# Kernel optimization log

Hardware: AMD Instinct MI355X
Metric: run time of the kernel (lower is better)

Reference implementation:

```python
import jax, jax.numpy as jnp
import numpy as np

TEMPERATURE = 8.0  # sqrt(d_k) with d_k = 64


def setup_inputs() -> dict:
    key = jax.random.key(0)
    kq, kk, kv, km = jax.random.split(key, 4)
    B, S, D = 32, 2048, 64
    q = jax.random.normal(kq, (B, S, D), dtype=jnp.float32)
    k = jax.random.normal(kk, (B, S, D), dtype=jnp.float32)
    v = jax.random.normal(kv, (B, S, D), dtype=jnp.float32)
    mask = jax.random.randint(km, (B, S, S), 0, 2).astype(jnp.bool_)
    return {"q": q, "k": k, "v": v, "mask": mask}


def reference(q, k, v, mask):
    # scores: [B, S, S] = q @ k^T, mask -> -inf, scale by 1/temperature
    scores = jnp.einsum("bqd,bkd->bqk", q, k)
    scores = jnp.where(mask, -jnp.inf, scores) / TEMPERATURE
    attn = jax.nn.softmax(scores, axis=2)
    output = jnp.einsum("bqk,bkd->bqd", attn, v)
    return (output, attn)
```

## Files before the change

kernel.cpp:

```cpp
#include <hip/hip_runtime.h>
#include <hip/hip_bf16.h>

typedef __attribute__((ext_vector_type(8))) short short8;
typedef __attribute__((ext_vector_type(4))) short short4b;
typedef __attribute__((ext_vector_type(4))) float f32x4;

#define S_LEN 2048
#define DIM   64
#define NB    32
#define BR    64
#define BC    64
#define NKT   (S_LEN / BC)

#define KP  72
#define BP  33
#define AP  68

__device__ __forceinline__ short f2bf(float f) {
    __hip_bfloat16 h = __float2bfloat16(f);
    return __builtin_bit_cast(short, h);
}

__device__ __forceinline__ void barrier_raw() {
    __builtin_amdgcn_sched_barrier(0);
    __builtin_amdgcn_s_barrier();
    __builtin_amdgcn_sched_barrier(0);
}
__device__ __forceinline__ void barrier_pub() {
    __builtin_amdgcn_sched_barrier(0);
    asm volatile("s_waitcnt lgkmcnt(0)" ::: "memory");
    __builtin_amdgcn_s_barrier();
    __builtin_amdgcn_sched_barrier(0);
}


__global__ __launch_bounds__(256)
void conv_k_kernel(const float* __restrict__ k, short* __restrict__ kbf)
{
    size_t idx = ((size_t)blockIdx.x * 256 + threadIdx.x) * 8;
    const float* p = k + idx;
    float4 a = *(const float4*)p;
    float4 c = *(const float4*)(p + 4);
    short8 f;
    f[0]=f2bf(a.x); f[1]=f2bf(a.y); f[2]=f2bf(a.z); f[3]=f2bf(a.w);
    f[4]=f2bf(c.x); f[5]=f2bf(c.y); f[6]=f2bf(c.z); f[7]=f2bf(c.w);
    *(short8*)(kbf + idx) = f;
}

__global__ __launch_bounds__(256)
void conv_vt_kernel(const float* __restrict__ v, short* __restrict__ vtb)
{
    __shared__ float tile[64][65];
    const int t  = threadIdx.x;
    const int b  = blockIdx.x >> 5;
    const int j0 = (blockIdx.x & 31) * 64;

    #pragma unroll
    for (int p = 0; p < 4; ++p) {
        int j = (t >> 4) + p * 16;
        int d = (t & 15) * 4;
        float4 x = *(const float4*)(v + ((size_t)(b * S_LEN + j0 + j) * DIM + d));
        tile[j][d+0]=x.x; tile[j][d+1]=x.y; tile[j][d+2]=x.z; tile[j][d+3]=x.w;
    }
    __syncthreads();
    #pragma unroll
    for (int p = 0; p < 4; ++p) {
        int d  = (t >> 4) + p * 16;
        int j4 = (t & 15) * 4;
        short4b s4;
        s4[0]=f2bf(tile[j4+0][d]); s4[1]=f2bf(tile[j4+1][d]);
        s4[2]=f2bf(tile[j4+2][d]); s4[3]=f2bf(tile[j4+3][d]);
        *(short4b*)(vtb + ((size_t)(b * DIM + d) * S_LEN + j0 + j4)) = s4;
    }
}


__global__ __launch_bounds__(256, 4)
void sdpa_v8(const float* __restrict__ q, const int* __restrict__ mask,
             const short* __restrict__ kbf, const short* __restrict__ vtb,
             float* __restrict__ out, float* __restrict__ attn)
{
    __shared__ __align__(16) short Klds[BR * KP];
    __shared__ __align__(16) short Vtlds[DIM * KP];
    __shared__ __align__(16) float Albs[BR * AP];

    const int t  = threadIdx.x;
    const int l  = t & 63;
    const int wv = t >> 6;
    const int lg = l >> 4;
    const int ll = l & 15;

    const int bx  = blockIdx.x;
    const int kk  = bx >> 3;
    const int b   = (bx & 7) * 4 + (kk >> 5);
    const int i0  = (kk & 31) * BR;

    const float LOG2E_T = 0.18033688011112042f;

    const int krow = t >> 2;
    const int kcol = (t & 3) * 16;
    const size_t kgbase = (size_t)(b * S_LEN + krow) * DIM + kcol;
    const size_t vgbase = (size_t)(b * DIM + krow) * S_LEN + kcol;
    const size_t mbase  = (size_t)(b * S_LEN + i0 + 16 * wv) * S_LEN + l;

    short8 qf[2];
    {
        const float* qrow = q + ((size_t)(b * S_LEN + i0 + 16 * wv + ll) * DIM);
        #pragma unroll
        for (int s = 0; s < 2; ++s) {
            const float* p = qrow + s * 32 + lg * 8;
            float4 a = *(const float4*)p;
            float4 c = *(const float4*)(p + 4);
            short8 f;
            f[0]=f2bf(a.x); f[1]=f2bf(a.y); f[2]=f2bf(a.z); f[3]=f2bf(a.w);
            f[4]=f2bf(c.x); f[5]=f2bf(c.y); f[6]=f2bf(c.z); f[7]=f2bf(c.w);
            qf[s] = f;
        }
    }

    short8 kA0 = *(const short8*)(kbf + kgbase);
    short8 kA1 = *(const short8*)(kbf + kgbase + 8);
    int mA[16], mB[16];
    #pragma unroll
    for (int r = 0; r < 16; ++r)
        mA[r] = __builtin_nontemporal_load(mask + mbase + (size_t)r * S_LEN);
    #pragma unroll
    for (int r = 0; r < 16; ++r)
        mB[r] = __builtin_nontemporal_load(mask + mbase + BC + (size_t)r * S_LEN);

    float rs[4] = {0.f, 0.f, 0.f, 0.f};
    unsigned long long w8[8];

    for (int o = 0; o < 4; ++o) {
        #pragma unroll
        for (int u = 0; u < 8; ++u) {
            const int kt = 8 * o + u;
            int (&cur)[16] = (u & 1) ? mB : mA;

            unsigned long long wb[4];
            #pragma unroll
            for (int r = 0; r < 16; ++r) {
                unsigned long long bal = __ballot(cur[r] != 0);
                if ((r >> 2) == lg) wb[r & 3] = bal;
                if (lg == o && ll == r) w8[u] = bal;
            }

            barrier_raw();
            {
                short* kd = &Klds[krow * KP + kcol];
                *(short8*)kd = kA0;
                *(short8*)(kd + 8) = kA1;
            }
            barrier_pub();

            {
                const int ktn = (kt < NKT - 1) ? kt + 1 : kt;
                const short* kb = kbf + kgbase + (size_t)ktn * BC * DIM;
                kA0 = *(const short8*)kb;
                kA1 = *(const short8*)(kb + 8);
                const int kt2 = (kt < NKT - 2) ? kt + 2 : kt;
                const int* mrow = mask + mbase + (size_t)kt2 * BC;
                #pragma unroll
                for (int r = 0; r < 16; ++r)
                    cur[r] = __builtin_nontemporal_load(mrow + (size_t)r * S_LEN);
            }
            __builtin_amdgcn_sched_barrier(0);

            #pragma unroll
            for (int jt = 0; jt < 4; ++jt) {
                short8 b0 = *(short8*)&Klds[(jt * 16 + ll) * KP + lg * 8];
                short8 b1 = *(short8*)&Klds[(jt * 16 + ll) * KP + 32 + lg * 8];
                f32x4 c = {0.f, 0.f, 0.f, 0.f};
                c = __builtin_amdgcn_mfma_f32_16x16x32_bf16(qf[0], b0, c, 0, 0, 0);
                c = __builtin_amdgcn_mfma_f32_16x16x32_bf16(qf[1], b1, c, 0, 0, 0);
                #pragma unroll
                for (int r = 0; r < 4; ++r) {
                    unsigned int bit = (unsigned int)(wb[r] >> (jt * 16 + ll)) & 1u;
                    rs[r] += bit ? 0.f : __builtin_amdgcn_exp2f(c[r] * LOG2E_T);
                }
            }
        }
    }

    kA0 = *(const short8*)(kbf + kgbase);
    kA1 = *(const short8*)(kbf + kgbase + 8);
    short8 vA0 = *(const short8*)(vtb + vgbase);
    short8 vA1 = *(const short8*)(vtb + vgbase + 8);

    float inv[4];
    #pragma unroll
    for (int r = 0; r < 4; ++r) {
        float s = rs[r];
        s += __shfl_xor(s, 1);
        s += __shfl_xor(s, 2);
        s += __shfl_xor(s, 4);
        s += __shfl_xor(s, 8);
        inv[r] = 1.0f / s;
    }

    f32x4 oacc[4];
    #pragma unroll
    for (int dt = 0; dt < 4; ++dt) oacc[dt] = (f32x4){0.f, 0.f, 0.f, 0.f};

    float* const abase = attn + (size_t)b * S_LEN * S_LEN;

    for (int o = 0; o < 4; ++o) {
        #pragma unroll
        for (int u = 0; u < 8; ++u) {
            const int kt = 8 * o + u;
            const int j0 = kt * BC;

            barrier_raw();
            {
                short* kd = &Klds[krow * KP + kcol];
                *(short8*)kd = kA0;
                *(short8*)(kd + 8) = kA1;
                short* vd = &Vtlds[krow * KP + kcol];
                *(short8*)vd = vA0;
                *(short8*)(vd + 8) = vA1;
            }
            barrier_pub();

            {
                const int ktn = (kt < NKT - 1) ? kt + 1 : kt;
                const short* kb = kbf + kgbase + (size_t)ktn * BC * DIM;
                kA0 = *(const short8*)kb;
                kA1 = *(const short8*)(kb + 8);
                const short* vb = vtb + vgbase + (size_t)ktn * BC;
                vA0 = *(const short8*)vb;
                vA1 = *(const short8*)(vb + 8);
            }
            __builtin_amdgcn_sched_barrier(0);

            unsigned long long wb[4];
            #pragma unroll
            for (int r = 0; r < 4; ++r)
                wb[r] = __shfl(w8[u], 16 * o + lg * 4 + r);

            #pragma unroll
            for (int jt = 0; jt < 4; ++jt) {
                short8 b0 = *(short8*)&Klds[(jt * 16 + ll) * KP + lg * 8];
                short8 b1 = *(short8*)&Klds[(jt * 16 + ll) * KP + 32 + lg * 8];
                f32x4 c = {0.f, 0.f, 0.f, 0.f};
                c = __builtin_amdgcn_mfma_f32_16x16x32_bf16(qf[0], b0, c, 0, 0, 0);
                c = __builtin_amdgcn_mfma_f32_16x16x32_bf16(qf[1], b1, c, 0, 0, 0);
                #pragma unroll
                for (int r = 0; r < 4; ++r) {
                    unsigned int bit = (unsigned int)(wb[r] >> (jt * 16 + ll)) & 1u;
                    float pexp = bit ? 0.f : __builtin_amdgcn_exp2f(c[r] * LOG2E_T);
                    Albs[(16 * wv + lg * 4 + r) * AP + jt * 16 + ll] = pexp * inv[r];
                }
            }

            short8 paf[2];
            #pragma unroll
            for (int s = 0; s < 2; ++s) {
                const float* ap = &Albs[(16 * wv + ll) * AP + s * 32 + lg * 8];
                float4 x = *(const float4*)ap;
                float4 y = *(const float4*)(ap + 4);
                short8 f;
                f[0]=f2bf(x.x); f[1]=f2bf(x.y); f[2]=f2bf(x.z); f[3]=f2bf(x.w);
                f[4]=f2bf(y.x); f[5]=f2bf(y.y); f[6]=f2bf(y.z); f[7]=f2bf(y.w);
                paf[s] = f;
            }

            #pragma unroll
            for (int dt = 0; dt < 4; ++dt) {
                short8 b0 = *(short8*)&Vtlds[(dt * 16 + ll) * KP + lg * 8];
                short8 b1 = *(short8*)&Vtlds[(dt * 16 + ll) * KP + 32 + lg * 8];
                oacc[dt] = __builtin_amdgcn_mfma_f32_16x16x32_bf16(paf[0], b0, oacc[dt], 0, 0, 0);
                oacc[dt] = __builtin_amdgcn_mfma_f32_16x16x32_bf16(paf[1], b1, oacc[dt], 0, 0, 0);
            }

            #pragma unroll
            for (int ps = 0; ps < 4; ++ps) {
                int row = 16 * wv + lg + ps * 4;
                f32x4 val = *(f32x4*)&Albs[row * AP + ll * 4];
                float* dst = abase + (size_t)(i0 + row) * S_LEN + j0 + ll * 4;
                __builtin_nontemporal_store(val, (f32x4*)dst);
            }
        }
    }

    #pragma unroll
    for (int dt = 0; dt < 4; ++dt)
        #pragma unroll
        for (int r = 0; r < 4; ++r)
            out[(size_t)(b * S_LEN + i0 + 16 * wv + lg * 4 + r) * DIM + dt * 16 + ll] = oacc[dt][r];
}


__global__ __launch_bounds__(256, 3)
void sdpa_fb(const float* __restrict__ q, const float* __restrict__ k,
             const float* __restrict__ v, const int* __restrict__ mask,
             float* __restrict__ out, float* __restrict__ attn)
{
    __shared__ __align__(16) short Klds[BR * KP];
    __shared__ __align__(16) short Vtlds[DIM * KP];
    __shared__ __align__(16) unsigned long long Bits[BR * BP];
    __shared__ __align__(16) float Albs[BR * AP];

    const int t  = threadIdx.x;
    const int l  = t & 63;
    const int wv = t >> 6;
    const int lg = l >> 4;
    const int ll = l & 15;

    const int wg = blockIdx.x;
    const int b  = wg >> 5;
    const int i0 = (wg & 31) * BR;

    const float LOG2E_T = 0.18033688011112042f;

    short8 qf[2];
    {
        const float* qrow = q + ((size_t)(b * S_LEN + i0 + 16 * wv + ll) * DIM);
        #pragma unroll
        for (int s = 0; s < 2; ++s) {
            const float* p = qrow + s * 32 + lg * 8;
            float4 a = *(const float4*)p;
            float4 c = *(const float4*)(p + 4);
            short8 f;
            f[0]=f2bf(a.x); f[1]=f2bf(a.y); f[2]=f2bf(a.z); f[3]=f2bf(a.w);
            f[4]=f2bf(c.x); f[5]=f2bf(c.y); f[6]=f2bf(c.z); f[7]=f2bf(c.w);
            qf[s] = f;
        }
    }

    float rs[4] = {0.f, 0.f, 0.f, 0.f};

    for (int kt = 0; kt < NKT; ++kt) {
        const int j0 = kt * BC;
        #pragma unroll
        for (int p = 0; p < 4; ++p) {
            int row = (t >> 4) + p * 16;
            int dd  = (t & 15) * 4;
            float4 kv4 = *(const float4*)(k + ((size_t)(b * S_LEN + j0 + row) * DIM + dd));
            short4b s4;
            s4[0]=f2bf(kv4.x); s4[1]=f2bf(kv4.y); s4[2]=f2bf(kv4.z); s4[3]=f2bf(kv4.w);
            *(short4b*)&Klds[row * KP + dd] = s4;
        }
        {
            const int* mrow = mask + (size_t)(b * S_LEN + i0 + 16 * wv) * S_LEN + j0 + l;
            int mv[16];
            #pragma unroll
            for (int r = 0; r < 16; ++r)
                mv[r] = __builtin_nontemporal_load(mrow + (size_t)r * S_LEN);
            unsigned long long myword = 0ull;
            #pragma unroll
            for (int r = 0; r < 16; ++r) {
                unsigned long long bal = __ballot(mv[r] != 0);
                if (ll == r) myword = bal;
            }
            if (l < 16) Bits[(16 * wv + l) * BP + kt] = myword;
        }
        __syncthreads();

        unsigned long long wbits[4];
        #pragma unroll
        for (int r = 0; r < 4; ++r)
            wbits[r] = Bits[(16 * wv + lg * 4 + r) * BP + kt];

        #pragma unroll
        for (int jt = 0; jt < 4; ++jt) {
            short8 b0 = *(short8*)&Klds[(jt * 16 + ll) * KP + lg * 8];
            short8 b1 = *(short8*)&Klds[(jt * 16 + ll) * KP + 32 + lg * 8];
            f32x4 c = {0.f, 0.f, 0.f, 0.f};
            c = __builtin_amdgcn_mfma_f32_16x16x32_bf16(qf[0], b0, c, 0, 0, 0);
            c = __builtin_amdgcn_mfma_f32_16x16x32_bf16(qf[1], b1, c, 0, 0, 0);
            #pragma unroll
            for (int r = 0; r < 4; ++r) {
                unsigned int bit = (unsigned int)(wbits[r] >> (jt * 16 + ll)) & 1u;
                rs[r] += bit ? 0.f : __builtin_amdgcn_exp2f(c[r] * LOG2E_T);
            }
        }
        __syncthreads();
    }

    float inv[4];
    #pragma unroll
    for (int r = 0; r < 4; ++r) {
        float s = rs[r];
        s += __shfl_xor(s, 1);
        s += __shfl_xor(s, 2);
        s += __shfl_xor(s, 4);
        s += __shfl_xor(s, 8);
        inv[r] = 1.0f / s;
    }

    f32x4 oacc[4];
    #pragma unroll
    for (int dt = 0; dt < 4; ++dt) oacc[dt] = (f32x4){0.f, 0.f, 0.f, 0.f};

    for (int kt = 0; kt < NKT; ++kt) {
        const int j0 = kt * BC;
        #pragma unroll
        for (int p = 0; p < 4; ++p) {
            int row = (t >> 4) + p * 16;
            int dd  = (t & 15) * 4;
            float4 kv4 = *(const float4*)(k + ((size_t)(b * S_LEN + j0 + row) * DIM + dd));
            short4b s4;
            s4[0]=f2bf(kv4.x); s4[1]=f2bf(kv4.y); s4[2]=f2bf(kv4.z); s4[3]=f2bf(kv4.w);
            *(short4b*)&Klds[row * KP + dd] = s4;
        }
        #pragma unroll
        for (int it = 0; it < 8; ++it) {
            int jp = (t >> 4) + (it & 1) * 16;
            int dd = (t & 15) + (it >> 1) * 16;
            const float* vp = v + ((size_t)(b * S_LEN + j0 + jp * 2) * DIM + dd);
            float v0 = vp[0];
            float v1 = vp[DIM];
            unsigned int pk = (unsigned int)(unsigned short)f2bf(v0) |
                              ((unsigned int)(unsigned short)f2bf(v1) << 16);
            *(unsigned int*)&Vtlds[dd * KP + jp * 2] = pk;
        }
        __syncthreads();

        unsigned long long wbits[4];
        #pragma unroll
        for (int r = 0; r < 4; ++r)
            wbits[r] = Bits[(16 * wv + lg * 4 + r) * BP + kt];

        #pragma unroll
        for (int jt = 0; jt < 4; ++jt) {
            short8 b0 = *(short8*)&Klds[(jt * 16 + ll) * KP + lg * 8];
            short8 b1 = *(short8*)&Klds[(jt * 16 + ll) * KP + 32 + lg * 8];
            f32x4 c = {0.f, 0.f, 0.f, 0.f};
            c = __builtin_amdgcn_mfma_f32_16x16x32_bf16(qf[0], b0, c, 0, 0, 0);
            c = __builtin_amdgcn_mfma_f32_16x16x32_bf16(qf[1], b1, c, 0, 0, 0);
            #pragma unroll
            for (int r = 0; r < 4; ++r) {
                unsigned int bit = (unsigned int)(wbits[r] >> (jt * 16 + ll)) & 1u;
                float pexp = bit ? 0.f : __builtin_amdgcn_exp2f(c[r] * LOG2E_T);
                Albs[(16 * wv + lg * 4 + r) * AP + jt * 16 + ll] = pexp * inv[r];
            }
        }

        short8 paf[2];
        #pragma unroll
        for (int s = 0; s < 2; ++s) {
            const float* ap = &Albs[(16 * wv + ll) * AP + s * 32 + lg * 8];
            float4 x = *(const float4*)ap;
            float4 y = *(const float4*)(ap + 4);
            short8 f;
            f[0]=f2bf(x.x); f[1]=f2bf(x.y); f[2]=f2bf(x.z); f[3]=f2bf(x.w);
            f[4]=f2bf(y.x); f[5]=f2bf(y.y); f[6]=f2bf(y.z); f[7]=f2bf(y.w);
            paf[s] = f;
        }

        #pragma unroll
        for (int dt = 0; dt < 4; ++dt) {
            short8 b0 = *(short8*)&Vtlds[(dt * 16 + ll) * KP + lg * 8];
            short8 b1 = *(short8*)&Vtlds[(dt * 16 + ll) * KP + 32 + lg * 8];
            oacc[dt] = __builtin_amdgcn_mfma_f32_16x16x32_bf16(paf[0], b0, oacc[dt], 0, 0, 0);
            oacc[dt] = __builtin_amdgcn_mfma_f32_16x16x32_bf16(paf[1], b1, oacc[dt], 0, 0, 0);
        }

        {
            float* abase = attn + (size_t)b * S_LEN * S_LEN;
            #pragma unroll
            for (int ps = 0; ps < 4; ++ps) {
                int row = 16 * wv + lg + ps * 4;
                f32x4 val = *(f32x4*)&Albs[row * AP + ll * 4];
                float* dst = abase + (size_t)(i0 + row) * S_LEN + j0 + ll * 4;
                __builtin_nontemporal_store(val, (f32x4*)dst);
            }
        }
        __syncthreads();
    }

    #pragma unroll
    for (int dt = 0; dt < 4; ++dt)
        #pragma unroll
        for (int r = 0; r < 4; ++r)
            out[(size_t)(b * S_LEN + i0 + 16 * wv + lg * 4 + r) * DIM + dt * 16 + ll] = oacc[dt][r];
}

extern "C" void kernel_launch(void* const* d_in, const int* in_sizes, int n_in,
                              void* d_out, int out_size, void* d_ws, size_t ws_size,
                              hipStream_t stream) {
    const float* q    = (const float*)d_in[0];
    const float* k    = (const float*)d_in[1];
    const float* v    = (const float*)d_in[2];
    const int*   mask = (const int*)d_in[3];
    float* out  = (float*)d_out;
    float* attn = out + (size_t)NB * S_LEN * DIM;

    const size_t nel = (size_t)NB * S_LEN * DIM;
    const size_t ws_needed = 2 * nel * sizeof(short);

    if (ws_size >= ws_needed) {
        short* kbf = (short*)d_ws;
        short* vtb = kbf + nel;
        conv_k_kernel<<<dim3(nel / (256 * 8)), dim3(256), 0, stream>>>(k, kbf);
        conv_vt_kernel<<<dim3(NB * 32), dim3(256), 0, stream>>>(v, vtb);
        sdpa_v8<<<dim3(NB * (S_LEN / BR)), dim3(256), 0, stream>>>(q, mask, kbf, vtb, out, attn);
    } else {
        sdpa_fb<<<dim3(NB * (S_LEN / BR)), dim3(256), 0, stream>>>(q, k, v, mask, out, attn);
    }
}
```

Before: 305.2 us.

## Process key tiles in pairs with explicit A/B register double-buffering

Both passes now step through the key dimension two 64-column tiles at a time, holding K (and V) prefetches in separate A/B register sets instead of reusing one set with a clamped index. The mask prefetch is restructured to load a 128-column strip (both halves) per step. In the output pass, the attn stores for both tiles are buffered in registers and written together as adjacent 128-column row segments. The aim is to keep more loads in flight and to coalesce the global attn writes, at the cost of higher register pressure under launch_bounds(256,4).

```diff
diff --git a/kernel.cpp b/kernel.cpp
--- a/kernel.cpp
+++ b/kernel.cpp
@@ -76,7 +76,7 @@
 
 
 __global__ __launch_bounds__(256, 4)
-void sdpa_v8(const float* __restrict__ q, const int* __restrict__ mask,
+void sdpa_v9(const float* __restrict__ q, const int* __restrict__ mask,
              const short* __restrict__ kbf, const short* __restrict__ vtb,
              float* __restrict__ out, float* __restrict__ attn)
 {
@@ -120,29 +120,32 @@
 
     short8 kA0 = *(const short8*)(kbf + kgbase);
     short8 kA1 = *(const short8*)(kbf + kgbase + 8);
-    int mA[16], mB[16];
-    #pragma unroll
-    for (int r = 0; r < 16; ++r)
-        mA[r] = __builtin_nontemporal_load(mask + mbase + (size_t)r * S_LEN);
-    #pragma unroll
-    for (int r = 0; r < 16; ++r)
-        mB[r] = __builtin_nontemporal_load(mask + mbase + BC + (size_t)r * S_LEN);
+    short8 kB0, kB1;
+    int m[32];
+    #pragma unroll
+    for (int r = 0; r < 16; ++r) {
+        m[2*r+0] = __builtin_nontemporal_load(mask + mbase + (size_t)r * S_LEN);
+        m[2*r+1] = __builtin_nontemporal_load(mask + mbase + (size_t)r * S_LEN + 64);
+    }
 
     float rs[4] = {0.f, 0.f, 0.f, 0.f};
     unsigned long long w8[8];
 
     for (int o = 0; o < 4; ++o) {
         #pragma unroll
-        for (int u = 0; u < 8; ++u) {
-            const int kt = 8 * o + u;
-            int (&cur)[16] = (u & 1) ? mB : mA;
-
-            unsigned long long wb[4];
+        for (int ss = 0; ss < 4; ++ss) {
+            const int kt0 = 8 * o + 2 * ss;
+            const int sI  = 4 * o + ss;
+
+            unsigned long long wb[2][4];
             #pragma unroll
             for (int r = 0; r < 16; ++r) {
-                unsigned long long bal = __ballot(cur[r] != 0);
-                if ((r >> 2) == lg) wb[r & 3] = bal;
-                if (lg == o && ll == r) w8[u] = bal;
+                #pragma unroll
+                for (int h = 0; h < 2; ++h) {
+                    unsigned long long bal = __ballot(m[2*r+h] != 0);
+                    if ((r >> 2) == lg) wb[h][r & 3] = bal;
+                    if (lg == o && ll == r) w8[2*ss+h] = bal;
+                }
             }
 
             barrier_raw();
@@ -152,20 +155,19 @@
                 *(short8*)(kd + 8) = kA1;
             }
             barrier_pub();
-
             {
-                const int ktn = (kt < NKT - 1) ? kt + 1 : kt;
-                const short* kb = kbf + kgbase + (size_t)ktn * BC * DIM;
-                kA0 = *(const short8*)kb;
-                kA1 = *(const short8*)(kb + 8);
-                const int kt2 = (kt < NKT - 2) ? kt + 2 : kt;
-                const int* mrow = mask + mbase + (size_t)kt2 * BC;
-                #pragma unroll
-                for (int r = 0; r < 16; ++r)
-                    cur[r] = __builtin_nontemporal_load(mrow + (size_t)r * S_LEN);
+                const short* kb = kbf + kgbase + (size_t)(kt0 + 1) * BC * DIM;
+                kB0 = *(const short8*)kb;
+                kB1 = *(const short8*)(kb + 8);
+                const int sN = (sI < 15) ? sI + 1 : sI;
+                const int* mp = mask + mbase + (size_t)sN * 128;
+                #pragma unroll
+                for (int r = 0; r < 16; ++r) {
+                    m[2*r+0] = __builtin_nontemporal_load(mp + (size_t)r * S_LEN);
+                    m[2*r+1] = __builtin_nontemporal_load(mp + (size_t)r * S_LEN + 64);
+                }
             }
             __builtin_amdgcn_sched_barrier(0);
-
             #pragma unroll
             for (int jt = 0; jt < 4; ++jt) {
                 short8 b0 = *(short8*)&Klds[(jt * 16 + ll) * KP + lg * 8];
@@ -175,7 +177,35 @@
                 c = __builtin_amdgcn_mfma_f32_16x16x32_bf16(qf[1], b1, c, 0, 0, 0);
                 #pragma unroll
                 for (int r = 0; r < 4; ++r) {
-                    unsigned int bit = (unsigned int)(wb[r] >> (jt * 16 + ll)) & 1u;
+                    unsigned int bit = (unsigned int)(wb[0][r] >> (jt * 16 + ll)) & 1u;
+                    rs[r] += bit ? 0.f : __builtin_amdgcn_exp2f(c[r] * LOG2E_T);
+                }
+            }
+
+            barrier_raw();
+            {
+                short* kd = &Klds[krow * KP + kcol];
+                *(short8*)kd = kB0;
+                *(short8*)(kd + 8) = kB1;
+            }
+            barrier_pub();
+            {
+                const int ktn = (kt0 + 2 < NKT) ? kt0 + 2 : NKT - 1;
+                const short* kb = kbf + kgbase + (size_t)ktn * BC * DIM;
+                kA0 = *(const short8*)kb;
+                kA1 = *(const short8*)(kb + 8);
+            }
+            __builtin_amdgcn_sched_barrier(0);
+            #pragma unroll
+            for (int jt = 0; jt < 4; ++jt) {
+                short8 b0 = *(short8*)&Klds[(jt * 16 + ll) * KP + lg * 8];
+                short8 b1 = *(short8*)&Klds[(jt * 16 + ll) * KP + 32 + lg * 8];
+                f32x4 c = {0.f, 0.f, 0.f, 0.f};
+                c = __builtin_amdgcn_mfma_f32_16x16x32_bf16(qf[0], b0, c, 0, 0, 0);
+                c = __builtin_amdgcn_mfma_f32_16x16x32_bf16(qf[1], b1, c, 0, 0, 0);
+                #pragma unroll
+                for (int r = 0; r < 4; ++r) {
+                    unsigned int bit = (unsigned int)(wb[1][r] >> (jt * 16 + ll)) & 1u;
                     rs[r] += bit ? 0.f : __builtin_amdgcn_exp2f(c[r] * LOG2E_T);
                 }
             }
@@ -186,6 +216,7 @@
     kA1 = *(const short8*)(kbf + kgbase + 8);
     short8 vA0 = *(const short8*)(vtb + vgbase);
     short8 vA1 = *(const short8*)(vtb + vgbase + 8);
+    short8 vB0, vB1;
 
     float inv[4];
     #pragma unroll
@@ -206,78 +237,95 @@
 
     for (int o = 0; o < 4; ++o) {
         #pragma unroll
-        for (int u = 0; u < 8; ++u) {
-            const int kt = 8 * o + u;
-            const int j0 = kt * BC;
-
-            barrier_raw();
-            {
-                short* kd = &Klds[krow * KP + kcol];
-                *(short8*)kd = kA0;
-                *(short8*)(kd + 8) = kA1;
-                short* vd = &Vtlds[krow * KP + kcol];
-                *(short8*)vd = vA0;
-                *(short8*)(vd + 8) = vA1;
-            }
-            barrier_pub();
-
-            {
-                const int ktn = (kt < NKT - 1) ? kt + 1 : kt;
-                const short* kb = kbf + kgbase + (size_t)ktn * BC * DIM;
-                kA0 = *(const short8*)kb;
-                kA1 = *(const short8*)(kb + 8);
-                const short* vb = vtb + vgbase + (size_t)ktn * BC;
-                vA0 = *(const short8*)vb;
-                vA1 = *(const short8*)(vb + 8);
-            }
-            __builtin_amdgcn_sched_barrier(0);
-
-            unsigned long long wb[4];
-            #pragma unroll
-            for (int r = 0; r < 4; ++r)
-                wb[r] = __shfl(w8[u], 16 * o + lg * 4 + r);
-
-            #pragma unroll
-            for (int jt = 0; jt < 4; ++jt) {
-                short8 b0 = *(short8*)&Klds[(jt * 16 + ll) * KP + lg * 8];
-                short8 b1 = *(short8*)&Klds[(jt * 16 + ll) * KP + 32 + lg * 8];
-                f32x4 c = {0.f, 0.f, 0.f, 0.f};
-                c = __builtin_amdgcn_mfma_f32_16x16x32_bf16(qf[0], b0, c, 0, 0, 0);
-                c = __builtin_amdgcn_mfma_f32_16x16x32_bf16(qf[1], b1, c, 0, 0, 0);
-                #pragma unroll
-                for (int r = 0; r < 4; ++r) {
-                    unsigned int bit = (unsigned int)(wb[r] >> (jt * 16 + ll)) & 1u;
-                    float pexp = bit ? 0.f : __builtin_amdgcn_exp2f(c[r] * LOG2E_T);
-                    Albs[(16 * wv + lg * 4 + r) * AP + jt * 16 + ll] = pexp * inv[r];
-                }
-            }
-
-            short8 paf[2];
-            #pragma unroll
-            for (int s = 0; s < 2; ++s) {
-                const float* ap = &Albs[(16 * wv + ll) * AP + s * 32 + lg * 8];
-                float4 x = *(const float4*)ap;
-                float4 y = *(const float4*)(ap + 4);
-                short8 f;
-                f[0]=f2bf(x.x); f[1]=f2bf(x.y); f[2]=f2bf(x.z); f[3]=f2bf(x.w);
-                f[4]=f2bf(y.x); f[5]=f2bf(y.y); f[6]=f2bf(y.z); f[7]=f2bf(y.w);
-                paf[s] = f;
-            }
-
-            #pragma unroll
-            for (int dt = 0; dt < 4; ++dt) {
-                short8 b0 = *(short8*)&Vtlds[(dt * 16 + ll) * KP + lg * 8];
-                short8 b1 = *(short8*)&Vtlds[(dt * 16 + ll) * KP + 32 + lg * 8];
-                oacc[dt] = __builtin_amdgcn_mfma_f32_16x16x32_bf16(paf[0], b0, oacc[dt], 0, 0, 0);
-                oacc[dt] = __builtin_amdgcn_mfma_f32_16x16x32_bf16(paf[1], b1, oacc[dt], 0, 0, 0);
+        for (int ss = 0; ss < 4; ++ss) {
+            const int kt0 = 8 * o + 2 * ss;
+            const int j0s = kt0 * BC;
+
+            f32x4 pst[2][4];
+
+            #pragma unroll
+            for (int h = 0; h < 2; ++h) {
+                barrier_raw();
+                {
+                    short* kd = &Klds[krow * KP + kcol];
+                    *(short8*)kd = (h ? kB0 : kA0);
+                    *(short8*)(kd + 8) = (h ? kB1 : kA1);
+                    short* vd = &Vtlds[krow * KP + kcol];
+                    *(short8*)vd = (h ? vB0 : vA0);
+                    *(short8*)(vd + 8) = (h ? vB1 : vA1);
+                }
+                barrier_pub();
+                if (h == 0) {
+                    const short* kb = kbf + kgbase + (size_t)(kt0 + 1) * BC * DIM;
+                    kB0 = *(const short8*)kb;
+                    kB1 = *(const short8*)(kb + 8);
+                    const short* vb = vtb + vgbase + (size_t)(kt0 + 1) * BC;
+                    vB0 = *(const short8*)vb;
+                    vB1 = *(const short8*)(vb + 8);
+                } else {
+                    const int ktn = (kt0 + 2 < NKT) ? kt0 + 2 : NKT - 1;
+                    const short* kb = kbf + kgbase + (size_t)ktn * BC * DIM;
+                    kA0 = *(const short8*)kb;
+                    kA1 = *(const short8*)(kb + 8);
+                    const short* vb = vtb + vgbase + (size_t)ktn * BC;
+                    vA0 = *(const short8*)vb;
+                    vA1 = *(const short8*)(vb + 8);
+                }
+                __builtin_amdgcn_sched_barrier(0);
+
+                unsigned long long wb[4];
+                #pragma unroll
+                for (int r = 0; r < 4; ++r)
+                    wb[r] = __shfl(w8[2*ss+h], 16 * o + lg * 4 + r);
+
+                #pragma unroll
+                for (int jt = 0; jt < 4; ++jt) {
+                    short8 b0 = *(short8*)&Klds[(jt * 16 + ll) * KP + lg * 8];
+                    short8 b1 = *(short8*)&Klds[(jt * 16 + ll) * KP + 32 + lg * 8];
+                    f32x4 c = {0.f, 0.f, 0.f, 0.f};
+                    c = __builtin_amdgcn_mfma_f32_16x16x32_bf16(qf[0], b0, c, 0, 0, 0);
+                    c = __builtin_amdgcn_mfma_f32_16x16x32_bf16(qf[1], b1, c, 0, 0, 0);
+                    #pragma unroll
+                    for (int r = 0; r < 4; ++r) {
+                        unsigned int bit = (unsigned int)(wb[r] >> (jt * 16 + ll)) & 1u;
+                        float pexp = bit ? 0.f : __builtin_amdgcn_exp2f(c[r] * LOG2E_T);
+                        Albs[(16 * wv + lg * 4 + r) * AP + jt * 16 + ll] = pexp * inv[r];
+                    }
+                }
+
+                short8 paf[2];
+                #pragma unroll
+                for (int s = 0; s < 2; ++s) {
+                    const float* ap = &Albs[(16 * wv + ll) * AP + s * 32 + lg * 8];
+                    float4 x = *(const float4*)ap;
+                    float4 y = *(const float4*)(ap + 4);
+                    short8 f;
+                    f[0]=f2bf(x.x); f[1]=f2bf(x.y); f[2]=f2bf(x.z); f[3]=f2bf(x.w);
+                    f[4]=f2bf(y.x); f[5]=f2bf(y.y); f[6]=f2bf(y.z); f[7]=f2bf(y.w);
+                    paf[s] = f;
+                }
+
+                #pragma unroll
+                for (int dt = 0; dt < 4; ++dt) {
+                    short8 b0 = *(short8*)&Vtlds[(dt * 16 + ll) * KP + lg * 8];
+                    short8 b1 = *(short8*)&Vtlds[(dt * 16 + ll) * KP + 32 + lg * 8];
+                    oacc[dt] = __builtin_amdgcn_mfma_f32_16x16x32_bf16(paf[0], b0, oacc[dt], 0, 0, 0);
+                    oacc[dt] = __builtin_amdgcn_mfma_f32_16x16x32_bf16(paf[1], b1, oacc[dt], 0, 0, 0);
+                }
+
+                #pragma unroll
+                for (int ps = 0; ps < 4; ++ps) {
+                    int row = 16 * wv + lg + ps * 4;
+                    pst[h][ps] = *(f32x4*)&Albs[row * AP + ll * 4];
+                }
             }
 
             #pragma unroll
             for (int ps = 0; ps < 4; ++ps) {
                 int row = 16 * wv + lg + ps * 4;
-                f32x4 val = *(f32x4*)&Albs[row * AP + ll * 4];
-                float* dst = abase + (size_t)(i0 + row) * S_LEN + j0 + ll * 4;
-                __builtin_nontemporal_store(val, (f32x4*)dst);
+                float* dst = abase + (size_t)(i0 + row) * S_LEN + j0s + ll * 4;
+                __builtin_nontemporal_store(pst[0][ps], (f32x4*)dst);
+                __builtin_nontemporal_store(pst[1][ps], (f32x4*)(dst + BC));
             }
         }
     }
@@ -494,7 +542,7 @@
         short* vtb = kbf + nel;
         conv_k_kernel<<<dim3(nel / (256 * 8)), dim3(256), 0, stream>>>(k, kbf);
         conv_vt_kernel<<<dim3(NB * 32), dim3(256), 0, stream>>>(v, vtb);
-        sdpa_v8<<<dim3(NB * (S_LEN / BR)), dim3(256), 0, stream>>>(q, mask, kbf, vtb, out, attn);
+        sdpa_v9<<<dim3(NB * (S_LEN / BR)), dim3(256), 0, stream>>>(q, mask, kbf, vtb, out, attn);
     } else {
         sdpa_fb<<<dim3(NB * (S_LEN / BR)), dim3(256), 0, stream>>>(q, k, v, mask, out, attn);
     }
```

Result: faster. 278.0 us (-8.9%).

## Preload mask bitmasks upfront and batch attn stores across two key tiles

Applied to the files above, without the earlier changes.

The mask is now read in one burst at kernel start: each wave loads 32 columns per row and converts them to ballot bitmasks stored in w8, instead of streaming mask tiles through double-buffered registers during pass one. Pass one then recovers its per-row bits with shuffles, as pass two already did. Pass two is unrolled over pairs of key tiles with ping-pong K/V register prefetch, and the attn values of both tiles are kept in registers and written together as wider contiguous row segments. This trades a large upfront latency burst and more register pressure for fewer in-loop mask loads and better-coalesced output writes.

```diff
diff --git a/kernel.cpp b/kernel.cpp
--- a/kernel.cpp
+++ b/kernel.cpp
@@ -76,9 +76,9 @@
 
 
 __global__ __launch_bounds__(256, 4)
-void sdpa_v8(const float* __restrict__ q, const int* __restrict__ mask,
-             const short* __restrict__ kbf, const short* __restrict__ vtb,
-             float* __restrict__ out, float* __restrict__ attn)
+void sdpa_v10(const float* __restrict__ q, const int* __restrict__ mask,
+              const short* __restrict__ kbf, const short* __restrict__ vtb,
+              float* __restrict__ out, float* __restrict__ attn)
 {
     __shared__ __align__(16) short Klds[BR * KP];
     __shared__ __align__(16) short Vtlds[DIM * KP];
@@ -101,7 +101,6 @@
     const int kcol = (t & 3) * 16;
     const size_t kgbase = (size_t)(b * S_LEN + krow) * DIM + kcol;
     const size_t vgbase = (size_t)(b * DIM + krow) * S_LEN + kcol;
-    const size_t mbase  = (size_t)(b * S_LEN + i0 + 16 * wv) * S_LEN + l;
 
     short8 qf[2];
     {
@@ -118,32 +117,32 @@
         }
     }
 
+    unsigned long long w8[8];
+    {
+        const int* mrowbase = mask + (size_t)(b * S_LEN + i0 + 16 * wv) * S_LEN + l;
+        for (int r = 0; r < 16; ++r) {
+            const int* mrow = mrowbase + (size_t)r * S_LEN;
+            int mv[32];
+            #pragma unroll
+            for (int c = 0; c < 32; ++c)
+                mv[c] = __builtin_nontemporal_load(mrow + c * 64);
+            #pragma unroll
+            for (int c = 0; c < 32; ++c) {
+                unsigned long long bal = __ballot(mv[c] != 0);
+                if (lg == (c >> 3) && ll == r) w8[c & 7] = bal;
+            }
+        }
+    }
+
     short8 kA0 = *(const short8*)(kbf + kgbase);
     short8 kA1 = *(const short8*)(kbf + kgbase + 8);
-    int mA[16], mB[16];
-    #pragma unroll
-    for (int r = 0; r < 16; ++r)
-        mA[r] = __builtin_nontemporal_load(mask + mbase + (size_t)r * S_LEN);
-    #pragma unroll
-    for (int r = 0; r < 16; ++r)
-        mB[r] = __builtin_nontemporal_load(mask + mbase + BC + (size_t)r * S_LEN);
 
     float rs[4] = {0.f, 0.f, 0.f, 0.f};
-    unsigned long long w8[8];
 
     for (int o = 0; o < 4; ++o) {
         #pragma unroll
         for (int u = 0; u < 8; ++u) {
             const int kt = 8 * o + u;
-            int (&cur)[16] = (u & 1) ? mB : mA;
-
-            unsigned long long wb[4];
-            #pragma unroll
-            for (int r = 0; r < 16; ++r) {
-                unsigned long long bal = __ballot(cur[r] != 0);
-                if ((r >> 2) == lg) wb[r & 3] = bal;
-                if (lg == o && ll == r) w8[u] = bal;
-            }
 
             barrier_raw();
             {
@@ -158,13 +157,13 @@
                 const short* kb = kbf + kgbase + (size_t)ktn * BC * DIM;
                 kA0 = *(const short8*)kb;
                 kA1 = *(const short8*)(kb + 8);
-                const int kt2 = (kt < NKT - 2) ? kt + 2 : kt;
-                const int* mrow = mask + mbase + (size_t)kt2 * BC;
-                #pragma unroll
-                for (int r = 0; r < 16; ++r)
-                    cur[r] = __builtin_nontemporal_load(mrow + (size_t)r * S_LEN);
             }
             __builtin_amdgcn_sched_barrier(0);
+
+            unsigned long long wb[4];
+            #pragma unroll
+            for (int r = 0; r < 4; ++r)
+                wb[r] = __shfl(w8[u], 16 * o + lg * 4 + r);
 
             #pragma unroll
             for (int jt = 0; jt < 4; ++jt) {
@@ -186,6 +185,7 @@
     kA1 = *(const short8*)(kbf + kgbase + 8);
     short8 vA0 = *(const short8*)(vtb + vgbase);
     short8 vA1 = *(const short8*)(vtb + vgbase + 8);
+    short8 kB0, kB1, vB0, vB1;
 
     float inv[4];
     #pragma unroll
@@ -206,78 +206,95 @@
 
     for (int o = 0; o < 4; ++o) {
         #pragma unroll
-        for (int u = 0; u < 8; ++u) {
-            const int kt = 8 * o + u;
-            const int j0 = kt * BC;
-
-            barrier_raw();
-            {
-                short* kd = &Klds[krow * KP + kcol];
-                *(short8*)kd = kA0;
-                *(short8*)(kd + 8) = kA1;
-                short* vd = &Vtlds[krow * KP + kcol];
-                *(short8*)vd = vA0;
-                *(short8*)(vd + 8) = vA1;
-            }
-            barrier_pub();
-
-            {
-                const int ktn = (kt < NKT - 1) ? kt + 1 : kt;
-                const short* kb = kbf + kgbase + (size_t)ktn * BC * DIM;
-                kA0 = *(const short8*)kb;
-                kA1 = *(const short8*)(kb + 8);
-                const short* vb = vtb + vgbase + (size_t)ktn * BC;
-                vA0 = *(const short8*)vb;
-                vA1 = *(const short8*)(vb + 8);
-            }
-            __builtin_amdgcn_sched_barrier(0);
-
-            unsigned long long wb[4];
-            #pragma unroll
-            for (int r = 0; r < 4; ++r)
-                wb[r] = __shfl(w8[u], 16 * o + lg * 4 + r);
-
-            #pragma unroll
-            for (int jt = 0; jt < 4; ++jt) {
-                short8 b0 = *(short8*)&Klds[(jt * 16 + ll) * KP + lg * 8];
-                short8 b1 = *(short8*)&Klds[(jt * 16 + ll) * KP + 32 + lg * 8];
-                f32x4 c = {0.f, 0.f, 0.f, 0.f};
-                c = __builtin_amdgcn_mfma_f32_16x16x32_bf16(qf[0], b0, c, 0, 0, 0);
-                c = __builtin_amdgcn_mfma_f32_16x16x32_bf16(qf[1], b1, c, 0, 0, 0);
+        for (int ss = 0; ss < 4; ++ss) {
+            const int kt0 = 8 * o + 2 * ss;
+            const int j0s = kt0 * BC;
+
+            f32x4 pst[2][4];
+
+            #pragma unroll
+            for (int h = 0; h < 2; ++h) {
+                barrier_raw();
+                {
+                    short* kd = &Klds[krow * KP + kcol];
+                    *(short8*)kd = (h ? kB0 : kA0);
+                    *(short8*)(kd + 8) = (h ? kB1 : kA1);
+                    short* vd = &Vtlds[krow * KP + kcol];
+                    *(short8*)vd = (h ? vB0 : vA0);
+                    *(short8*)(vd + 8) = (h ? vB1 : vA1);
+                }
+                barrier_pub();
+                if (h == 0) {
+                    const short* kb = kbf + kgbase + (size_t)(kt0 + 1) * BC * DIM;
+                    kB0 = *(const short8*)kb;
+                    kB1 = *(const short8*)(kb + 8);
+                    const short* vb = vtb + vgbase + (size_t)(kt0 + 1) * BC;
+                    vB0 = *(const short8*)vb;
+                    vB1 = *(const short8*)(vb + 8);
+                } else {
+                    const int ktn = (kt0 + 2 < NKT) ? kt0 + 2 : NKT - 1;
+                    const short* kb = kbf + kgbase + (size_t)ktn * BC * DIM;
+                    kA0 = *(const short8*)kb;
+                    kA1 = *(const short8*)(kb + 8);
+                    const short* vb = vtb + vgbase + (size_t)ktn * BC;
+                    vA0 = *(const short8*)vb;
+                    vA1 = *(const short8*)(vb + 8);
+                }
+                __builtin_amdgcn_sched_barrier(0);
+
+                unsigned long long wb[4];
                 #pragma unroll
-                for (int r = 0; r < 4; ++r) {
-                    unsigned int bit = (unsigned int)(wb[r] >> (jt * 16 + ll)) & 1u;
-                    float pexp = bit ? 0.f : __builtin_amdgcn_exp2f(c[r] * LOG2E_T);
-                    Albs[(16 * wv + lg * 4 + r) * AP + jt * 16 + ll] = pexp * inv[r];
-                }
-            }
-
-            short8 paf[2];
-            #pragma unroll
-            for (int s = 0; s < 2; ++s) {
-                const float* ap = &Albs[(16 * wv + ll) * AP + s * 32 + lg * 8];
-                float4 x = *(const float4*)ap;
-                float4 y = *(const float4*)(ap + 4);
-                short8 f;
-                f[0]=f2bf(x.x); f[1]=f2bf(x.y); f[2]=f2bf(x.z); f[3]=f2bf(x.w);
-                f[4]=f2bf(y.x); f[5]=f2bf(y.y); f[6]=f2bf(y.z); f[7]=f2bf(y.w);
-                paf[s] = f;
-            }
-
-            #pragma unroll
-            for (int dt = 0; dt < 4; ++dt) {
-                short8 b0 = *(short8*)&Vtlds[(dt * 16 + ll) * KP + lg * 8];
-                short8 b1 = *(short8*)&Vtlds[(dt * 16 + ll) * KP + 32 + lg * 8];
-                oacc[dt] = __builtin_amdgcn_mfma_f32_16x16x32_bf16(paf[0], b0, oacc[dt], 0, 0, 0);
-                oacc[dt] = __builtin_amdgcn_mfma_f32_16x16x32_bf16(paf[1], b1, oacc[dt], 0, 0, 0);
+                for (int r = 0; r < 4; ++r)
+                    wb[r] = __shfl(w8[2 * ss + h], 16 * o + lg * 4 + r);
+
+                #pragma unroll
+                for (int jt = 0; jt < 4; ++jt) {
+                    short8 b0 = *(short8*)&Klds[(jt * 16 + ll) * KP + lg * 8];
+                    short8 b1 = *(short8*)&Klds[(jt * 16 + ll) * KP + 32 + lg * 8];
+                    f32x4 c = {0.f, 0.f, 0.f, 0.f};
+                    c = __builtin_amdgcn_mfma_f32_16x16x32_bf16(qf[0], b0, c, 0, 0, 0);
+                    c = __builtin_amdgcn_mfma_f32_16x16x32_bf16(qf[1], b1, c, 0, 0, 0);
+                    #pragma unroll
+                    for (int r = 0; r < 4; ++r) {
+                        unsigned int bit = (unsigned int)(wb[r] >> (jt * 16 + ll)) & 1u;
+                        float pexp = bit ? 0.f : __builtin_amdgcn_exp2f(c[r] * LOG2E_T);
+                        Albs[(16 * wv + lg * 4 + r) * AP + jt * 16 + ll] = pexp * inv[r];
+                    }
+                }
+
+                short8 paf[2];
+                #pragma unroll
+                for (int s = 0; s < 2; ++s) {
+                    const float* ap = &Albs[(16 * wv + ll) * AP + s * 32 + lg * 8];
+                    float4 x = *(const float4*)ap;
+                    float4 y = *(const float4*)(ap + 4);
+                    short8 f;
+                    f[0]=f2bf(x.x); f[1]=f2bf(x.y); f[2]=f2bf(x.z); f[3]=f2bf(x.w);
+                    f[4]=f2bf(y.x); f[5]=f2bf(y.y); f[6]=f2bf(y.z); f[7]=f2bf(y.w);
+                    paf[s] = f;
+                }
+
+                #pragma unroll
+                for (int dt = 0; dt < 4; ++dt) {
+                    short8 b0 = *(short8*)&Vtlds[(dt * 16 + ll) * KP + lg * 8];
+                    short8 b1 = *(short8*)&Vtlds[(dt * 16 + ll) * KP + 32 + lg * 8];
+                    oacc[dt] = __builtin_amdgcn_mfma_f32_16x16x32_bf16(paf[0], b0, oacc[dt], 0, 0, 0);
+                    oacc[dt] = __builtin_amdgcn_mfma_f32_16x16x32_bf16(paf[1], b1, oacc[dt], 0, 0, 0);
+                }
+
+                #pragma unroll
+                for (int ps = 0; ps < 4; ++ps) {
+                    int row = 16 * wv + lg + ps * 4;
+                    pst[h][ps] = *(f32x4*)&Albs[row * AP + ll * 4];
+                }
             }
 
             #pragma unroll
             for (int ps = 0; ps < 4; ++ps) {
                 int row = 16 * wv + lg + ps * 4;
-                f32x4 val = *(f32x4*)&Albs[row * AP + ll * 4];
-                float* dst = abase + (size_t)(i0 + row) * S_LEN + j0 + ll * 4;
-                __builtin_nontemporal_store(val, (f32x4*)dst);
+                float* dst = abase + (size_t)(i0 + row) * S_LEN + j0s + ll * 4;
+                __builtin_nontemporal_store(pst[0][ps], (f32x4*)dst);
+                __builtin_nontemporal_store(pst[1][ps], (f32x4*)(dst + BC));
             }
         }
     }
@@ -494,7 +511,7 @@
         short* vtb = kbf + nel;
         conv_k_kernel<<<dim3(nel / (256 * 8)), dim3(256), 0, stream>>>(k, kbf);
         conv_vt_kernel<<<dim3(NB * 32), dim3(256), 0, stream>>>(v, vtb);
-        sdpa_v8<<<dim3(NB * (S_LEN / BR)), dim3(256), 0, stream>>>(q, mask, kbf, vtb, out, attn);
+        sdpa_v10<<<dim3(NB * (S_LEN / BR)), dim3(256), 0, stream>>>(q, mask, kbf, vtb, out, attn);
     } else {
         sdpa_fb<<<dim3(NB * (S_LEN / BR)), dim3(256), 0, stream>>>(q, k, v, mask, out, attn);
     }
```

After: 284.9 us. -6.7%, faster.
